# Kernel optimization log

Measured on AMD Instinct MI355X. Metric: run time of the kernel, lower is better.

Reference implementation:

```python
import jax, jax.numpy as jnp
import numpy as np

N = 4096
IN_F = 256
H = 8
F = 64  # out_features per head
ALPHA = 0.2
NEG_BIG = -9e15


def setup_inputs() -> dict:
    key = jax.random.key(0)
    k1, k2, k3, k4 = jax.random.split(key, 4)
    h = jax.random.normal(k1, (N, IN_F), dtype=jnp.float32)
    adj = jax.random.randint(k2, (N, N), 0, 2, dtype=jnp.int32)
    W = jax.random.normal(k3, (IN_F, H * F), dtype=jnp.float32) * (1.0 / np.sqrt(IN_F))
    a = jax.random.normal(k4, (H, 2 * F), dtype=jnp.float32) * (1.0 / np.sqrt(2 * F))
    bias = jnp.zeros((H * F,), dtype=jnp.float32)
    return {"h": h, "adj": adj, "W": W, "a": a, "bias": bias}


def reference(h, adj, W, a, bias):
    n = h.shape[0]
    Wh = (h @ W).reshape(n, H, F)               # [N,H,F]
    a1 = a[:, :F]                                # [H,F]
    a2 = a[:, F:]                                # [H,F]
    attn_1 = jnp.einsum('nhf,hf->nh', Wh, a1)    # [N,H]
    attn_2 = jnp.einsum('nhf,hf->nh', Wh, a2)    # [N,H]
    e = jax.nn.leaky_relu(attn_1[:, None, :] + attn_2[None, :, :], negative_slope=ALPHA)  # [N,N,H]
    e = jnp.where(adj[..., None] > 0, e, NEG_BIG)
    attn = jax.nn.softmax(e, axis=1)             # softmax over source nodes j
    h_prime = jnp.einsum('ijh,jhf->ihf', attn, Wh)  # [N,H,F]
    return h_prime.reshape(n, H * F) + bias
```

## Files before the change

### kernel.cpp

```cpp
#include <hip/hip_runtime.h>
#include <hip/hip_bf16.h>

typedef __bf16 bf16;
typedef __attribute__((ext_vector_type(4)))  __bf16 bf16x4;
typedef __attribute__((ext_vector_type(8)))  __bf16 bf16x8;
typedef __attribute__((ext_vector_type(4)))  float  f32x4;
typedef __attribute__((ext_vector_type(16))) float  f32x16;

#define NN   4096
#define INF  256
#define HH   8
#define FF   64
#define HF   512
#define ALPHA_ 0.2f
#define NW   128


__global__ __launch_bounds__(256) void k_pack(const int* __restrict__ adj,
                                              unsigned* __restrict__ bits)
{
    const int t   = blockIdx.x * 256 + threadIdx.x;
    const int row = t >> 7;
    const int jw  = t & 127;
    const int* p  = adj + (size_t)row * NN + (jw << 5);
    unsigned m = 0u;
#pragma unroll
    for (int k = 0; k < 8; ++k) {
        const int4 v = *(const int4*)(p + (k << 2));
        m |= (v.x != 0 ? 1u : 0u) << (4 * k);
        m |= (v.y != 0 ? 1u : 0u) << (4 * k + 1);
        m |= (v.z != 0 ? 1u : 0u) << (4 * k + 2);
        m |= (v.w != 0 ? 1u : 0u) << (4 * k + 3);
    }
    bits[t] = m;
}

__global__ __launch_bounds__(256) void k_wht(const float* __restrict__ A,
                                             const float* __restrict__ W,
                                             bf16* __restrict__ WhTt)
{
    __shared__ bf16 Bs[64][36];
    const int bid = blockIdx.x;
    const int mt = (bid >> 3) << 6;
    const int nt = (bid & 7) << 6;
    const int tid = threadIdx.x;
    const int wv  = tid >> 6;
    const int l   = tid & 63;
    const int l15 = l & 15;
    const int lq  = l >> 4;

    f32x4 acc[4];
#pragma unroll
    for (int nb = 0; nb < 4; ++nb) acc[nb] = (f32x4)0.0f;

    const int krow = tid >> 3;
    const int ncol = (tid & 7) << 3;

    for (int kb = 0; kb < INF; kb += 32) {
        const float4 w0 = *(const float4*)&W[(kb + krow) * HF + nt + ncol];
        const float4 w1 = *(const float4*)&W[(kb + krow) * HF + nt + ncol + 4];
        __syncthreads();
        Bs[ncol + 0][krow] = (bf16)w0.x; Bs[ncol + 1][krow] = (bf16)w0.y;
        Bs[ncol + 2][krow] = (bf16)w0.z; Bs[ncol + 3][krow] = (bf16)w0.w;
        Bs[ncol + 4][krow] = (bf16)w1.x; Bs[ncol + 5][krow] = (bf16)w1.y;
        Bs[ncol + 6][krow] = (bf16)w1.z; Bs[ncol + 7][krow] = (bf16)w1.w;
        __syncthreads();

        const float* pA = A + (mt + wv * 16 + l15) * INF + kb + (lq << 2);
        const float4 a0 = *(const float4*)pA;
        const float4 a1 = *(const float4*)(pA + 16);
        bf16x8 af;
        af[0] = (bf16)a0.x; af[1] = (bf16)a0.y; af[2] = (bf16)a0.z; af[3] = (bf16)a0.w;
        af[4] = (bf16)a1.x; af[5] = (bf16)a1.y; af[6] = (bf16)a1.z; af[7] = (bf16)a1.w;

#pragma unroll
        for (int nb = 0; nb < 4; ++nb) {
            const bf16* pB = &Bs[(nb << 4) + l15][lq << 2];
            bf16x4 blo = *(const bf16x4*)pB;
            bf16x4 bhi = *(const bf16x4*)(pB + 16);
            bf16x8 bf = __builtin_shufflevector(blo, bhi, 0,1,2,3,4,5,6,7);
            acc[nb] = __builtin_amdgcn_mfma_f32_16x16x32_bf16(af, bf, acc[nb], 0, 0, 0);
        }
    }

    const int m0 = mt + wv * 16 + (lq << 2);
#pragma unroll
    for (int nb = 0; nb < 4; ++nb) {
        const int col = nt + (nb << 4) + l15;
        bf16x4 o;
#pragma unroll
        for (int r = 0; r < 4; ++r) o[r] = (bf16)acc[nb][r];
        const int hd_ = col >> 6, row_ = col & 63;
        bf16* dst = WhTt + (((size_t)(hd_ << 8) + (m0 >> 4)) << 10)
                  + (row_ << 4) + (m0 & 15);
        *(bf16x4*)dst = o;
    }
}

__global__ __launch_bounds__(256) void k_scores(const bf16* __restrict__ WhTt,
                                                const float* __restrict__ a,
                                                float* __restrict__ E1, float* __restrict__ F1,
                                                bf16* __restrict__ E2b, bf16* __restrict__ F2b)
{
    const int h = blockIdx.x >> 4;
    const int i = ((blockIdx.x & 15) << 8) + threadIdx.x;
    const bf16* wb = WhTt + (((size_t)(h << 8) + (i >> 4)) << 10) + (i & 15);
    float t1 = 0.f, t2 = 0.f;
#pragma unroll 16
    for (int f = 0; f < FF; ++f) {
        float w = (float)wb[f << 4];
        t1 += w * a[h * 128 + f];
        t2 += w * a[h * 128 + 64 + f];
    }
    E1[h * NN + i]  = __expf(t1);
    F1[h * NN + i]  = __expf(ALPHA_ * t1);
    E2b[h * NN + i] = (bf16)__expf(t2);
    F2b[h * NN + i] = (bf16)__expf(ALPHA_ * t2);
}

#define DECL_STAGE(P) \
    unsigned P##_bw; \
    bf16x8 P##_ea, P##_fa, P##_b0, P##_b1;

#define LOAD_STAGE(P, s) do { \
    const int jb_ = jwb + ((s) << 4); \
    const bf16* tb_ = whb + ((s) << 10); \
    P##_bw = (unsigned)bitrow16[(s)]; \
    P##_ea = *(const bf16x8*)(e2r + jb_); \
    P##_fa = *(const bf16x8*)(f2r + jb_); \
    P##_b0 = *(const bf16x8*)(tb_ + (l31 << 4) + (lh << 3)); \
    P##_b1 = *(const bf16x8*)(tb_ + ((32 + l31) << 4) + (lh << 3)); \
} while (0)

#define COMPUTE_STAGE(P) do { \
    const unsigned bsel_ = (P##_bw >> sh0) & 0xffu; \
    bf16x8 pa_; \
    _Pragma("unroll") \
    for (int k_ = 0; k_ < 8; ++k_) { \
        float w_ = ((bsel_ >> k_) & 1u) \
                 ? fmaxf(e1 * (float)P##_ea[k_], f1 * (float)P##_fa[k_]) : 0.f; \
        den += w_; pa_[k_] = (bf16)w_; \
    } \
    acc0 = __builtin_amdgcn_mfma_f32_32x32x16_bf16(pa_, P##_b0, acc0, 0, 0, 0); \
    acc1 = __builtin_amdgcn_mfma_f32_32x32x16_bf16(pa_, P##_b1, acc1, 0, 0, 0); \
} while (0)

__global__ __launch_bounds__(512, 3) void k_gat(const unsigned* __restrict__ bits,
                                                const bf16* __restrict__ WhTt,
                                                const float* __restrict__ E1, const float* __restrict__ F1,
                                                const bf16* __restrict__ E2b, const bf16* __restrict__ F2b,
                                                const float* __restrict__ bias,
                                                float* __restrict__ out)
{
    __shared__ float red[4][32][64];
    __shared__ float dred[8][32];

    const int bid = blockIdx.x;
    const int hd = bid & 7;
    const int ib = bid >> 3;

    const int tid = threadIdx.x;
    const int wv  = tid >> 6;
    const int l   = tid & 63;
    const int l31 = l & 31;
    const int lh  = l >> 5;

    const int i = (ib << 5) + l31;

    const float e1 = E1[hd * NN + i];
    const float f1 = F1[hd * NN + i];

    f32x16 acc0 = (f32x16)0.f, acc1 = (f32x16)0.f;
    float den = 0.f;

    const unsigned short* bitrow16 =
        (const unsigned short*)(bits + (size_t)i * NW) + (wv << 5);
    const bf16* e2r = E2b + hd * NN;
    const bf16* f2r = F2b + hd * NN;
    const bf16* whb = WhTt + ((size_t)hd << 18) + ((size_t)(wv << 5) << 10);

    const int jwb = (wv << 9) + (lh << 3);
    const int sh0 = lh << 3;

    DECL_STAGE(A); DECL_STAGE(B);

    LOAD_STAGE(A, 0);
#pragma unroll 1
    for (int t = 0; t < 15; ++t) {
        LOAD_STAGE(B, 2 * t + 1); COMPUTE_STAGE(A);
        LOAD_STAGE(A, 2 * t + 2); COMPUTE_STAGE(B);
    }
    LOAD_STAGE(B, 31); COMPUTE_STAGE(A); COMPUTE_STAGE(B);

    den += __shfl_xor(den, 32, 64);
    if (l < 32) dred[wv][l31] = den;

    if (wv < 4) {
        float* rb = &red[wv][0][0];
#pragma unroll
        for (int g = 0; g < 4; ++g) {
            const int ir = (g << 3) + (lh << 2);
#pragma unroll
            for (int r = 0; r < 4; ++r) {
                rb[(ir + r) * 64 + l31     ] = acc0[4*g + r];
                rb[(ir + r) * 64 + 32 + l31] = acc1[4*g + r];
            }
        }
    }
    __syncthreads();
    if (wv >= 4) {
        float* rb = &red[wv - 4][0][0];
#pragma unroll
        for (int g = 0; g < 4; ++g) {
            const int ir = (g << 3) + (lh << 2);
#pragma unroll
            for (int r = 0; r < 4; ++r) {
                rb[(ir + r) * 64 + l31     ] += acc0[4*g + r];
                rb[(ir + r) * 64 + 32 + l31] += acc1[4*g + r];
            }
        }
    }
    __syncthreads();

    const int iloc = tid >> 4;
    const int c0   = (tid & 15) << 2;
    const float dsum = dred[0][iloc] + dred[1][iloc] + dred[2][iloc] + dred[3][iloc]
                     + dred[4][iloc] + dred[5][iloc] + dred[6][iloc] + dred[7][iloc];
    const float rd = 1.0f / dsum;
    f32x4 o;
#pragma unroll
    for (int r = 0; r < 4; ++r) {
        const float sv = red[0][iloc][c0 + r] + red[1][iloc][c0 + r]
                       + red[2][iloc][c0 + r] + red[3][iloc][c0 + r];
        o[r] = sv * rd + bias[(hd << 6) + c0 + r];
    }
    *(f32x4*)&out[(size_t)((ib << 5) + iloc) * HF + (hd << 6) + c0] = o;
}

extern "C" void kernel_launch(void* const* d_in, const int* in_sizes, int n_in,
                              void* d_out, int out_size, void* d_ws, size_t ws_size,
                              hipStream_t stream) {
    const float* h    = (const float*)d_in[0];
    const int*   adj  = (const int*)d_in[1];
    const float* W    = (const float*)d_in[2];
    const float* a    = (const float*)d_in[3];
    const float* bias = (const float*)d_in[4];
    float* out = (float*)d_out;

    char* ws = (char*)d_ws;
    bf16*     WhTt = (bf16*)ws;
    float*    E1   = (float*)(ws + (size_t)(4 << 20));
    float*    F1   = E1 + HH * NN;
    bf16*     E2b  = (bf16*)(F1 + HH * NN);
    bf16*     F2b  = E2b + HH * NN;
    unsigned* bits = (unsigned*)(ws + (size_t)(4 << 20) + (384 << 10));

    hipLaunchKernelGGL(k_pack,   dim3(2048), dim3(256), 0, stream, adj, bits);
    hipLaunchKernelGGL(k_wht,    dim3(512),  dim3(256), 0, stream, h, W, WhTt);
    hipLaunchKernelGGL(k_scores, dim3(128),  dim3(256), 0, stream, WhTt, a, E1, F1, E2b, F2b);
    hipLaunchKernelGGL(k_gat,    dim3(1024), dim3(512), 0, stream, bits, WhTt, E1, F1, E2b, F2b, bias, out);
}
```

Before: 90.61 us.

## Mask attention weights via bitwise LUT, compute denominator with MFMA, shrink LDS reduction

The per-element conditional select is replaced by computing all weights, converting them to bf16, then ANDing pairs with a shared-memory LUT of 16-bit masks. The denominator is accumulated by a third MFMA against an all-ones vector instead of scalar adds, which also makes it sum the same rounded bf16 weights used in the numerator. The cross-wave reduction buffer is halved (2 slots instead of 4) at the cost of more sequential __syncthreads phases, likely to cut LDS footprint and raise occupancy. The extra MFMA adds matrix-core work and accumulator registers per stage.

Result: faster. 83.85 us (-7.5%).

```diff
diff --git a/kernel.cpp b/kernel.cpp
--- a/kernel.cpp
+++ b/kernel.cpp
@@ -6,6 +6,7 @@
 typedef __attribute__((ext_vector_type(8)))  __bf16 bf16x8;
 typedef __attribute__((ext_vector_type(4)))  float  f32x4;
 typedef __attribute__((ext_vector_type(16))) float  f32x16;
+typedef __attribute__((ext_vector_type(4)))  unsigned u32x4;
 
 #define NN   4096
 #define INF  256
@@ -137,12 +138,16 @@
     bf16x8 pa_; \
     _Pragma("unroll") \
     for (int k_ = 0; k_ < 8; ++k_) { \
-        float w_ = ((bsel_ >> k_) & 1u) \
-                 ? fmaxf(e1 * (float)P##_ea[k_], f1 * (float)P##_fa[k_]) : 0.f; \
-        den += w_; pa_[k_] = (bf16)w_; \
+        const float w_ = fmaxf(e1 * (float)P##_ea[k_], f1 * (float)P##_fa[k_]); \
+        pa_[k_] = (bf16)w_; \
     } \
+    u32x4 pm_ = __builtin_bit_cast(u32x4, pa_); \
+    _Pragma("unroll") \
+    for (int d_ = 0; d_ < 4; ++d_) pm_[d_] &= lut4[(bsel_ >> (2 * d_)) & 3u]; \
+    pa_ = __builtin_bit_cast(bf16x8, pm_); \
     acc0 = __builtin_amdgcn_mfma_f32_32x32x16_bf16(pa_, P##_b0, acc0, 0, 0, 0); \
     acc1 = __builtin_amdgcn_mfma_f32_32x32x16_bf16(pa_, P##_b1, acc1, 0, 0, 0); \
+    accd = __builtin_amdgcn_mfma_f32_32x32x16_bf16(pa_, ones, accd, 0, 0, 0); \
 } while (0)
 
 __global__ __launch_bounds__(512, 3) void k_gat(const unsigned* __restrict__ bits,
@@ -152,8 +157,9 @@
                                                 const float* __restrict__ bias,
                                                 float* __restrict__ out)
 {
-    __shared__ float red[4][32][64];
+    __shared__ float red2[2][32][64];
     __shared__ float dred[8][32];
+    __shared__ unsigned lut4[4];
 
     const int bid = blockIdx.x;
     const int hd = bid & 7;
@@ -165,13 +171,19 @@
     const int l31 = l & 31;
     const int lh  = l >> 5;
 
+    if (tid < 4) lut4[tid] = (tid & 1 ? 0x0000FFFFu : 0u) | (tid & 2 ? 0xFFFF0000u : 0u);
+    __syncthreads();
+
     const int i = (ib << 5) + l31;
 
     const float e1 = E1[hd * NN + i];
     const float f1 = F1[hd * NN + i];
 
-    f32x16 acc0 = (f32x16)0.f, acc1 = (f32x16)0.f;
-    float den = 0.f;
+    f32x16 acc0 = (f32x16)0.f, acc1 = (f32x16)0.f, accd = (f32x16)0.f;
+
+    bf16x8 ones;
+#pragma unroll
+    for (int k = 0; k < 8; ++k) ones[k] = (bf16)1.0f;
 
     const unsigned short* bitrow16 =
         (const unsigned short*)(bits + (size_t)i * NW) + (wv << 5);
@@ -192,11 +204,15 @@
     }
     LOAD_STAGE(B, 31); COMPUTE_STAGE(A); COMPUTE_STAGE(B);
 
-    den += __shfl_xor(den, 32, 64);
-    if (l < 32) dred[wv][l31] = den;
-
-    if (wv < 4) {
-        float* rb = &red[wv][0][0];
+    if (l31 == 0) {
+#pragma unroll
+        for (int r = 0; r < 16; ++r) {
+            dred[wv][(r & 3) + 8 * (r >> 2) + 4 * lh] = accd[r];
+        }
+    }
+
+    if (wv < 2) {
+        float* rb = &red2[wv][0][0];
 #pragma unroll
         for (int g = 0; g < 4; ++g) {
             const int ir = (g << 3) + (lh << 2);
@@ -208,8 +224,34 @@
         }
     }
     __syncthreads();
-    if (wv >= 4) {
-        float* rb = &red[wv - 4][0][0];
+    if (wv == 2 || wv == 3) {
+        float* rb = &red2[wv - 2][0][0];
+#pragma unroll
+        for (int g = 0; g < 4; ++g) {
+            const int ir = (g << 3) + (lh << 2);
+#pragma unroll
+            for (int r = 0; r < 4; ++r) {
+                rb[(ir + r) * 64 + l31     ] += acc0[4*g + r];
+                rb[(ir + r) * 64 + 32 + l31] += acc1[4*g + r];
+            }
+        }
+    }
+    __syncthreads();
+    if (wv == 4 || wv == 5) {
+        float* rb = &red2[wv - 4][0][0];
+#pragma unroll
+        for (int g = 0; g < 4; ++g) {
+            const int ir = (g << 3) + (lh << 2);
+#pragma unroll
+            for (int r = 0; r < 4; ++r) {
+                rb[(ir + r) * 64 + l31     ] += acc0[4*g + r];
+                rb[(ir + r) * 64 + 32 + l31] += acc1[4*g + r];
+            }
+        }
+    }
+    __syncthreads();
+    if (wv == 6 || wv == 7) {
+        float* rb = &red2[wv - 6][0][0];
 #pragma unroll
         for (int g = 0; g < 4; ++g) {
             const int ir = (g << 3) + (lh << 2);
@@ -230,8 +272,7 @@
     f32x4 o;
 #pragma unroll
     for (int r = 0; r < 4; ++r) {
-        const float sv = red[0][iloc][c0 + r] + red[1][iloc][c0 + r]
-                       + red[2][iloc][c0 + r] + red[3][iloc][c0 + r];
+        const float sv = red2[0][iloc][c0 + r] + red2[1][iloc][c0 + r];
         o[r] = sv * rd + bias[(hd << 6) + c0 + r];
     }
     *(f32x4*)&out[(size_t)((ib << 5) + iloc) * HF + (hd << 6) + c0] = o;
```
